# Kernel optimization log

Hardware: AMD Instinct MI355X
Metric: run time of the kernel (lower is better)

The kernel has to match this reference:

```python
import jax, jax.numpy as jnp
import numpy as np

D_MODEL = 1024
N_HEADS = 16
D_K = D_MODEL // N_HEADS
THETA = 10000.0
NEG_INF = -1e30


def _rope_tables(token_positions, d_k, theta=THETA):
    # freqs[t, i] = t / theta**(2i/d_k), i in [0, d_k/2)
    exponent = jnp.arange(0, d_k, 2, dtype=jnp.float32)  # [d_k/2]
    inv_freq = 1.0 / theta ** (exponent / d_k)
    freqs = token_positions.astype(jnp.float32)[:, None] * inv_freq[None, :]  # [s, d_k/2]
    return jnp.cos(freqs), jnp.sin(freqs)


def _apply_rope(x, cos, sin):
    # x: [..., s, d_k]; interleaved pair rotation (pairs are (x[2i], x[2i+1]))
    x1 = x[..., 0::2]
    x2 = x[..., 1::2]
    r1 = x1 * cos - x2 * sin
    r2 = x1 * sin + x2 * cos
    return jnp.stack([r1, r2], axis=-1).reshape(x.shape)


def setup_inputs() -> dict:
    key = jax.random.key(0)
    ks = jax.random.split(key, 5)
    b, s = 2, 2048
    scale = np.sqrt(2.0 / (D_MODEL + D_MODEL))
    return {
        "x": jax.random.normal(ks[0], (b, s, D_MODEL), dtype=jnp.float32),
        "Wq": jax.random.normal(ks[1], (D_MODEL, D_MODEL), dtype=jnp.float32) * scale,
        "Wk": jax.random.normal(ks[2], (D_MODEL, D_MODEL), dtype=jnp.float32) * scale,
        "Wv": jax.random.normal(ks[3], (D_MODEL, D_MODEL), dtype=jnp.float32) * scale,
        "Wo": jax.random.normal(ks[4], (D_MODEL, D_MODEL), dtype=jnp.float32) * scale,
        "token_positions": jnp.arange(s, dtype=jnp.int64 if jax.config.jax_enable_x64 else jnp.int32),
    }


def reference(x, Wq, Wk, Wv, Wo, token_positions):
    b, s, _ = x.shape
    # QKV projections: weight stored [in, out]
    q = jnp.einsum('bsi,io->bso', x, Wq)
    k = jnp.einsum('bsi,io->bso', x, Wk)
    v = jnp.einsum('bsi,io->bso', x, Wv)
    # split heads: [b, h, s, d_k]
    q = q.reshape(b, s, N_HEADS, D_K).transpose(0, 2, 1, 3)
    k = k.reshape(b, s, N_HEADS, D_K).transpose(0, 2, 1, 3)
    v = v.reshape(b, s, N_HEADS, D_K).transpose(0, 2, 1, 3)
    # RoPE
    cos, sin = _rope_tables(token_positions, D_K)
    q = _apply_rope(q, cos, sin)
    k = _apply_rope(k, cos, sin)
    # causal attention with full materialized scores (faithful to source)
    scores = jnp.einsum('bhid,bhjd->bhij', q, k) / jnp.sqrt(jnp.float32(D_K))
    mask = jnp.tril(jnp.ones((s, s), dtype=bool))
    scores = jnp.where(mask, scores, NEG_INF)
    probs = jax.nn.softmax(scores, axis=-1)
    out = jnp.einsum('bhij,bhjd->bhid', probs, v)
    out = out.transpose(0, 2, 1, 3).reshape(b, s, D_MODEL)
    return jnp.einsum('bsi,io->bso', out, Wo)
```

## Files before the change

### kernel.cpp

```cpp
#include <hip/hip_runtime.h>
#include <cmath>

#define S_LEN 2048
#define DMODEL 1024
#define NHEADS 16
#define DK 64
#define BATCH 2
#define MTOT (BATCH * S_LEN)

using short8 = __attribute__((ext_vector_type(8))) short;
using floatx4 = __attribute__((ext_vector_type(4))) float;

__device__ __forceinline__ unsigned short f2b(float f) {
    union { float f; unsigned u; } v; v.f = f;
    unsigned r = v.u + 0x7fff + ((v.u >> 16) & 1);
    return (unsigned short)(r >> 16);
}

__device__ __forceinline__ void gload16(const void* g, void* l) {
    __builtin_amdgcn_global_load_lds(
        (const __attribute__((address_space(1))) unsigned int*)g,
        (__attribute__((address_space(3))) unsigned int*)l, 16, 0, 0);
}

__global__ void rope_tables_k(const int* __restrict__ tokpos,
                              float* __restrict__ ct, float* __restrict__ st) {
    int idx = blockIdx.x * blockDim.x + threadIdx.x;
    int si = idx >> 5;
    int ip = idx & 31;
    float pos = (float)tokpos[si];
    float inv_freq = powf(10000.0f, -(float)(2 * ip) / 64.0f);
    float ang = pos * inv_freq;
    ct[idx] = cosf(ang);
    st[idx] = sinf(ang);
}

__global__ __launch_bounds__(256) void cast_x_k(const float* __restrict__ x,
                                                unsigned short* __restrict__ xb) {
    int i = (blockIdx.x * 256 + threadIdx.x) * 8;
    float4 a = *(const float4*)(x + i);
    float4 b = *(const float4*)(x + i + 4);
    short8 o;
    o[0] = f2b(a.x); o[1] = f2b(a.y); o[2] = f2b(a.z); o[3] = f2b(a.w);
    o[4] = f2b(b.x); o[5] = f2b(b.y); o[6] = f2b(b.z); o[7] = f2b(b.w);
    *(short8*)(xb + i) = o;
}

__global__ __launch_bounds__(256) void trans_w_k(
    const float* W0, const float* W1, const float* W2, const float* W3,
    unsigned short* T0, unsigned short* T1, unsigned short* T2, unsigned short* T3) {
    __shared__ float t[64][65];
    int z = blockIdx.z;
    const float* W = z == 0 ? W0 : z == 1 ? W1 : z == 2 ? W2 : W3;
    unsigned short* T = z == 0 ? T0 : z == 1 ? T1 : z == 2 ? T2 : T3;
    const bool perm = (z < 2);
    int n0 = blockIdx.x * 64, k0 = blockIdx.y * 64;
    int rr = threadIdx.x >> 6, cc = threadIdx.x & 63;
#pragma unroll
    for (int r = 0; r < 16; r++) {
        int row = r * 4 + rr;
        t[row][cc] = W[(size_t)(k0 + row) * DMODEL + n0 + cc];
    }
    __syncthreads();
#pragma unroll
    for (int r = 0; r < 16; r++) {
        int row = r * 4 + rr;
        int drow = perm ? (((row & 1) ? 32 : 0) + (row >> 1)) : row;
        T[(size_t)(n0 + drow) * DMODEL + k0 + cc] = f2b(t[cc][row]);
    }
}

__global__ __launch_bounds__(256) void vtrans_k(const unsigned short* __restrict__ V,
                                                unsigned short* __restrict__ Vt) {
    __shared__ unsigned short t[64][72];
    const int tid = threadIdx.x;
    const int s0 = blockIdx.x * 64, d0 = blockIdx.y * 64;
    const int bb = s0 >> 11;
#pragma unroll
    for (int it = 0; it < 4; it++) {
        int e = (it * 256 + tid) * 4;
        int r = e >> 6, c = e & 63;
        *(ushort4*)&t[r][c] = *(const ushort4*)(V + (size_t)(s0 + r) * DMODEL + d0 + c);
    }
    __syncthreads();
#pragma unroll
    for (int it = 0; it < 4; it++) {
        int e = (it * 256 + tid) * 4;
        int r = e >> 6, c = e & 63;
        ushort4 v;
        v.x = t[c + 0][r]; v.y = t[c + 1][r];
        v.z = t[c + 2][r]; v.w = t[c + 3][r];
        *(ushort4*)(Vt + (size_t)(bb * 1024 + d0 + r) * S_LEN + (s0 & (S_LEN - 1)) + c) = v;
    }
}

__global__ __launch_bounds__(256) void mm_k(
    const unsigned short* __restrict__ A,
    const unsigned short* __restrict__ Bt0, const unsigned short* __restrict__ Bt1,
    const unsigned short* __restrict__ Bt2,
    void* C0, void* C1, void* C2,
    const float* __restrict__ ct, const float* __restrict__ st, int kind) {
    __shared__ __align__(16) unsigned short blob[8192];

    const int z = blockIdx.z;
    const unsigned short* Bt = z == 0 ? Bt0 : z == 1 ? Bt1 : Bt2;
    void* C = z == 0 ? C0 : z == 1 ? C1 : C2;
    const int mode = (kind == 1) ? 0 : (z == 2 ? 3 : 1);

    const int tid = threadIdx.x;
    const int w = tid >> 6, lane = tid & 63;
    const int l15 = lane & 15, quad = lane >> 4;
    const int wr = w >> 1, wc = w & 1;
    const int m0 = blockIdx.y * 128, n0 = blockIdx.x * 128;

    floatx4 acc[4][4];
#pragma unroll
    for (int i = 0; i < 4; i++)
#pragma unroll
        for (int j = 0; j < 4; j++) acc[i][j] = (floatx4){0.f, 0.f, 0.f, 0.f};

    for (int k0 = 0; k0 < DMODEL; k0 += 32) {
        if (k0) __syncthreads();
#pragma unroll
        for (int it = 0; it < 4; it++) {
            int g = it * 4 + w;
            const unsigned short* gp;
            if (g < 8)
                gp = A + (size_t)(m0 + g * 16 + l15) * DMODEL + k0 + (lane >> 4) * 8;
            else
                gp = Bt + (size_t)(n0 + (g - 8) * 16 + l15) * DMODEL + k0 + (lane >> 4) * 8;
            gload16(gp, (char*)blob + g * 1024);
        }
        __syncthreads();

        short8 af[4], bfr[4];
#pragma unroll
        for (int i = 0; i < 4; i++)
            af[i] = *(const short8*)((char*)blob + ((wr * 4 + i) * 64 + lane) * 16);
#pragma unroll
        for (int j = 0; j < 4; j++)
            bfr[j] = *(const short8*)((char*)blob + 8192 + ((wc * 4 + j) * 64 + lane) * 16);
#pragma unroll
        for (int i = 0; i < 4; i++)
#pragma unroll
            for (int j = 0; j < 4; j++)
                acc[i][j] = __builtin_amdgcn_mfma_f32_16x16x32_bf16(af[i], bfr[j], acc[i][j], 0, 0, 0);
    }

#pragma unroll
    for (int i = 0; i < 4; i++) {
        const int rowb = m0 + wr * 64 + i * 16 + quad * 4;
        if (mode == 0) {
            float* Cf = (float*)C;
#pragma unroll
            for (int j = 0; j < 4; j++) {
                int colb = n0 + wc * 64 + j * 16 + l15;
#pragma unroll
                for (int r = 0; r < 4; r++)
                    Cf[(size_t)(rowb + r) * DMODEL + colb] = acc[i][j][r];
            }
        } else if (mode == 1) {
            unsigned short* Cb = (unsigned short*)C;
#pragma unroll
            for (int jh = 0; jh < 2; jh++) {
                int ip = jh * 16 + l15;
                int cole = n0 + wc * 64 + jh * 16 + l15;
#pragma unroll
                for (int r = 0; r < 4; r++) {
                    int row = rowb + r;
                    int si = row & (S_LEN - 1);
                    float c = ct[si * 32 + ip];
                    float s = st[si * 32 + ip];
                    float e = acc[i][jh][r];
                    float od = acc[i][jh + 2][r];
                    Cb[(size_t)row * DMODEL + cole] = f2b(e * c - od * s);
                    Cb[(size_t)row * DMODEL + cole + 32] = f2b(e * s + od * c);
                }
            }
        } else {
            unsigned short* Cb = (unsigned short*)C;
#pragma unroll
            for (int j = 0; j < 4; j++) {
                int colb = n0 + wc * 64 + j * 16 + l15;
#pragma unroll
                for (int r = 0; r < 4; r++)
                    Cb[(size_t)(rowb + r) * DMODEL + colb] = f2b(acc[i][j][r]);
            }
        }
    }
}

__global__ __launch_bounds__(256) void attn_k(const unsigned short* __restrict__ Q,
                                              const unsigned short* __restrict__ K,
                                              const unsigned short* __restrict__ Vt,
                                              unsigned short* __restrict__ O) {
    __shared__ __align__(16) unsigned short Kblob[2][4096];
    __shared__ __align__(16) unsigned short Vblob[2][4096];
    __shared__ __align__(16) unsigned short Ps[4][16 * 72];

    const int tid = threadIdx.x;
    const int w = tid >> 6, lane = tid & 63;
    const int l15 = lane & 15, quad = lane >> 4;
    const int idx = blockIdx.x;
    const int qt = 31 - (idx >> 5);
    const int bh = idx & 31;
    const int bb = bh >> 4, h = bh & 15;
    const int qbase = qt * 64 + w * 16;
    const int qrow = qbase + l15;

    const size_t qoff = (size_t)(bb * S_LEN + qbase + l15) * DMODEL + h * DK;
    short8 aq0 = *(const short8*)(Q + qoff + quad * 8);
    short8 aq1 = *(const short8*)(Q + qoff + 32 + quad * 8);

    floatx4 o[4];
#pragma unroll
    for (int f = 0; f < 4; f++) o[f] = (floatx4){0.f, 0.f, 0.f, 0.f};
    float mv = -1e30f, lv = 0.f;

    const unsigned short* Kb = K + (size_t)(bb * S_LEN) * DMODEL + h * DK;
    const unsigned short* Vb = Vt + (size_t)(bb * 1024 + h * DK) * S_LEN;
    unsigned short* ps = &Ps[w][0];

    auto stage = [&](int b, int kb) {
#pragma unroll
        for (int it = 0; it < 4; it++) {
            int g = it * 4 + w;
            if (g < 8) {
                const unsigned short* gp =
                    Kb + (size_t)(kb + (g >> 1) * 16 + l15) * DMODEL + (g & 1) * 32 + quad * 8;
                gload16(gp, (char*)&Kblob[b][0] + g * 1024);
            } else {
                int gv = g - 8;
                const unsigned short* gp =
                    Vb + (size_t)((gv >> 1) * 16 + l15) * S_LEN + kb + (gv & 1) * 32 + quad * 8;
                gload16(gp, (char*)&Vblob[b][0] + gv * 1024);
            }
        }
    };

    const int nkt = qt + 1;
    stage(0, 0);
    for (int kt = 0; kt < nkt; kt++) {
        const int b = kt & 1;
        const int kb = kt * 64;
        __syncthreads();
        if (kt + 1 < nkt) stage(b ^ 1, (kt + 1) * 64);

        const unsigned short* kbb = &Kblob[b][0];
        floatx4 c[4];
#pragma unroll
        for (int g = 0; g < 4; g++) {
            short8 kf0 = *(const short8*)(kbb + (g * 2 + 0) * 512 + lane * 8);
            short8 kf1 = *(const short8*)(kbb + (g * 2 + 1) * 512 + lane * 8);
            floatx4 t = {0.f, 0.f, 0.f, 0.f};
            t = __builtin_amdgcn_mfma_f32_16x16x32_bf16(kf0, aq0, t, 0, 0, 0);
            c[g] = __builtin_amdgcn_mfma_f32_16x16x32_bf16(kf1, aq1, t, 0, 0, 0);
        }

        float sv[16];
#pragma unroll
        for (int g = 0; g < 4; g++)
#pragma unroll
            for (int r = 0; r < 4; r++) {
                int key = kb + g * 16 + quad * 4 + r;
                sv[g * 4 + r] = (key <= qrow) ? c[g][r] * 0.125f : -1e30f;
            }
        float mx = sv[0];
#pragma unroll
        for (int i = 1; i < 16; i++) mx = fmaxf(mx, sv[i]);
        mx = fmaxf(mx, __shfl_xor(mx, 16));
        mx = fmaxf(mx, __shfl_xor(mx, 32));
        float mnew = fmaxf(mv, mx);
        float alpha = __expf(mv - mnew);
        mv = mnew;
        float p[16], psum = 0.f;
#pragma unroll
        for (int i = 0; i < 16; i++) {
            p[i] = __expf(sv[i] - mnew);
            psum += p[i];
        }
        lv = lv * alpha + psum;

#pragma unroll
        for (int g = 0; g < 4; g++) {
            ushort4 pk;
            pk.x = f2b(p[g * 4 + 0]); pk.y = f2b(p[g * 4 + 1]);
            pk.z = f2b(p[g * 4 + 2]); pk.w = f2b(p[g * 4 + 3]);
            *(ushort4*)(ps + l15 * 72 + g * 16 + quad * 4) = pk;
        }
#pragma unroll
        for (int f = 0; f < 4; f++) {
            o[f][0] *= alpha; o[f][1] *= alpha;
            o[f][2] *= alpha; o[f][3] *= alpha;
        }
        short8 pf0 = *(const short8*)(ps + l15 * 72 + quad * 8);
        short8 pf1 = *(const short8*)(ps + l15 * 72 + 32 + quad * 8);
        const unsigned short* vbb = &Vblob[b][0];
#pragma unroll
        for (int f = 0; f < 4; f++) {
            short8 vf0 = *(const short8*)(vbb + (f * 2 + 0) * 512 + lane * 8);
            short8 vf1 = *(const short8*)(vbb + (f * 2 + 1) * 512 + lane * 8);
            o[f] = __builtin_amdgcn_mfma_f32_16x16x32_bf16(vf0, pf0, o[f], 0, 0, 0);
            o[f] = __builtin_amdgcn_mfma_f32_16x16x32_bf16(vf1, pf1, o[f], 0, 0, 0);
        }
    }

    lv += __shfl_xor(lv, 16);
    lv += __shfl_xor(lv, 32);
    float inv = 1.0f / lv;
    __syncthreads();
#pragma unroll
    for (int f = 0; f < 4; f++) {
        ushort4 pk;
        pk.x = f2b(o[f][0] * inv);
        pk.y = f2b(o[f][1] * inv);
        pk.z = f2b(o[f][2] * inv);
        pk.w = f2b(o[f][3] * inv);
        *(ushort4*)(ps + l15 * 72 + f * 16 + quad * 4) = pk;
    }
    short8 r0 = *(const short8*)(ps + l15 * 72 + quad * 8);
    short8 r1 = *(const short8*)(ps + l15 * 72 + 32 + quad * 8);
    size_t obase = (size_t)(bb * S_LEN + qbase + l15) * DMODEL + h * DK;
    *(short8*)(O + obase + quad * 8) = r0;
    *(short8*)(O + obase + 32 + quad * 8) = r1;
}

extern "C" void kernel_launch(void* const* d_in, const int* in_sizes, int n_in,
                              void* d_out, int out_size, void* d_ws,
                              size_t ws_size, hipStream_t stream) {
    const float* x = (const float*)d_in[0];
    const float* Wq = (const float*)d_in[1];
    const float* Wk = (const float*)d_in[2];
    const float* Wv = (const float*)d_in[3];
    const float* Wo = (const float*)d_in[4];
    const int* tokpos = (const int*)d_in[5];
    float* out = (float*)d_out;

    const size_t MD = (size_t)MTOT * DMODEL;
    const size_t WD = (size_t)DMODEL * DMODEL;
    unsigned short* xb = (unsigned short*)d_ws;
    unsigned short* Wqt = xb + MD;
    unsigned short* Wkt = Wqt + WD;
    unsigned short* Wvt = Wkt + WD;
    unsigned short* Wot = Wvt + WD;
    unsigned short* Q = Wot + WD;
    unsigned short* K = Q + MD;
    unsigned short* V = K + MD;
    unsigned short* Vt = V + MD;
    float* ct = (float*)(Vt + MD);
    float* st = ct + S_LEN * 32;
    unsigned short* O = V;

    rope_tables_k<<<dim3((S_LEN * 32) / 256), dim3(256), 0, stream>>>(tokpos, ct, st);
    cast_x_k<<<dim3(MD / 2048), dim3(256), 0, stream>>>(x, xb);
    trans_w_k<<<dim3(16, 16, 4), dim3(256), 0, stream>>>(Wq, Wk, Wv, Wo, Wqt, Wkt, Wvt, Wot);

    mm_k<<<dim3(8, 32, 3), dim3(256), 0, stream>>>(xb, Wqt, Wkt, Wvt,
                                                   (void*)Q, (void*)K, (void*)V, ct, st, 0);
    vtrans_k<<<dim3(64, 16), dim3(256), 0, stream>>>(V, Vt);
    attn_k<<<dim3(1024), dim3(256), 0, stream>>>(Q, K, Vt, O);
    mm_k<<<dim3(8, 32, 1), dim3(256), 0, stream>>>(O, Wot, Wot, Wot,
                                                   (void*)out, (void*)out, (void*)out, ct, st, 1);
}
```

Baseline: 224.0 us.

## Merge prep kernels, deepen GEMM K-step, and widen attention blocks to 128 queries

Three preprocessing kernels (rope tables, x cast, weight transpose) are folded into one launch that branches on block index, removing launch overhead. The GEMM stages a 64-wide K slice per iteration instead of 32, halving barriers and doubling LDS per block. Attention blocks grow to 512 threads covering 128 query rows, so each staged K/V tile is shared by eight waves instead of four. The cost is lower occupancy from the larger LDS and blocks, coarser causal load balance across 512 blocks, and the hidden attention loop body must handle diagonal masking for the 128-row tile correctly.

```diff
diff --git a/kernel.cpp b/kernel.cpp
--- a/kernel.cpp
+++ b/kernel.cpp
@@ -23,50 +23,51 @@
         (__attribute__((address_space(3))) unsigned int*)l, 16, 0, 0);
 }
 
-__global__ void rope_tables_k(const int* __restrict__ tokpos,
-                              float* __restrict__ ct, float* __restrict__ st) {
-    int idx = blockIdx.x * blockDim.x + threadIdx.x;
-    int si = idx >> 5;
-    int ip = idx & 31;
-    float pos = (float)tokpos[si];
-    float inv_freq = powf(10000.0f, -(float)(2 * ip) / 64.0f);
-    float ang = pos * inv_freq;
-    ct[idx] = cosf(ang);
-    st[idx] = sinf(ang);
-}
-
-__global__ __launch_bounds__(256) void cast_x_k(const float* __restrict__ x,
-                                                unsigned short* __restrict__ xb) {
-    int i = (blockIdx.x * 256 + threadIdx.x) * 8;
-    float4 a = *(const float4*)(x + i);
-    float4 b = *(const float4*)(x + i + 4);
-    short8 o;
-    o[0] = f2b(a.x); o[1] = f2b(a.y); o[2] = f2b(a.z); o[3] = f2b(a.w);
-    o[4] = f2b(b.x); o[5] = f2b(b.y); o[6] = f2b(b.z); o[7] = f2b(b.w);
-    *(short8*)(xb + i) = o;
-}
-
-__global__ __launch_bounds__(256) void trans_w_k(
+__global__ __launch_bounds__(256) void prep_k(
+    const float* __restrict__ x, unsigned short* __restrict__ xb,
+    const int* __restrict__ tokpos, float* __restrict__ ct, float* __restrict__ st,
     const float* W0, const float* W1, const float* W2, const float* W3,
     unsigned short* T0, unsigned short* T1, unsigned short* T2, unsigned short* T3) {
     __shared__ float t[64][65];
-    int z = blockIdx.z;
-    const float* W = z == 0 ? W0 : z == 1 ? W1 : z == 2 ? W2 : W3;
-    unsigned short* T = z == 0 ? T0 : z == 1 ? T1 : z == 2 ? T2 : T3;
-    const bool perm = (z < 2);
-    int n0 = blockIdx.x * 64, k0 = blockIdx.y * 64;
-    int rr = threadIdx.x >> 6, cc = threadIdx.x & 63;
-#pragma unroll
-    for (int r = 0; r < 16; r++) {
-        int row = r * 4 + rr;
-        t[row][cc] = W[(size_t)(k0 + row) * DMODEL + n0 + cc];
-    }
-    __syncthreads();
-#pragma unroll
-    for (int r = 0; r < 16; r++) {
-        int row = r * 4 + rr;
-        int drow = perm ? (((row & 1) ? 32 : 0) + (row >> 1)) : row;
-        T[(size_t)(n0 + drow) * DMODEL + k0 + cc] = f2b(t[cc][row]);
+    const int b = blockIdx.x;
+    if (b < 2048) {
+        int i = (b * 256 + threadIdx.x) * 8;
+        float4 a = *(const float4*)(x + i);
+        float4 bb = *(const float4*)(x + i + 4);
+        short8 o;
+        o[0] = f2b(a.x); o[1] = f2b(a.y); o[2] = f2b(a.z); o[3] = f2b(a.w);
+        o[4] = f2b(bb.x); o[5] = f2b(bb.y); o[6] = f2b(bb.z); o[7] = f2b(bb.w);
+        *(short8*)(xb + i) = o;
+    } else if (b < 2304) {
+        int idx = (b - 2048) * 256 + threadIdx.x;
+        int si = idx >> 5;
+        int ip = idx & 31;
+        float pos = (float)tokpos[si];
+        float inv_freq = powf(10000.0f, -(float)(2 * ip) / 64.0f);
+        float ang = pos * inv_freq;
+        ct[idx] = cosf(ang);
+        st[idx] = sinf(ang);
+    } else {
+        int id = b - 2304;
+        int z = id >> 8;
+        int bx = id & 15, by = (id >> 4) & 15;
+        const float* W = z == 0 ? W0 : z == 1 ? W1 : z == 2 ? W2 : W3;
+        unsigned short* T = z == 0 ? T0 : z == 1 ? T1 : z == 2 ? T2 : T3;
+        const bool perm = (z < 2);
+        int n0 = bx * 64, k0 = by * 64;
+        int rr = threadIdx.x >> 6, cc = threadIdx.x & 63;
+#pragma unroll
+        for (int r = 0; r < 16; r++) {
+            int row = r * 4 + rr;
+            t[row][cc] = W[(size_t)(k0 + row) * DMODEL + n0 + cc];
+        }
+        __syncthreads();
+#pragma unroll
+        for (int r = 0; r < 16; r++) {
+            int row = r * 4 + rr;
+            int drow = perm ? (((row & 1) ? 32 : 0) + (row >> 1)) : row;
+            T[(size_t)(n0 + drow) * DMODEL + k0 + cc] = f2b(t[cc][row]);
+        }
     }
 }
 
@@ -100,7 +101,7 @@
     const unsigned short* __restrict__ Bt2,
     void* C0, void* C1, void* C2,
     const float* __restrict__ ct, const float* __restrict__ st, int kind) {
-    __shared__ __align__(16) unsigned short blob[8192];
+    __shared__ __align__(16) unsigned short blob[16384];
 
     const int z = blockIdx.z;
     const unsigned short* Bt = z == 0 ? Bt0 : z == 1 ? Bt1 : Bt2;
@@ -119,32 +120,37 @@
 #pragma unroll
         for (int j = 0; j < 4; j++) acc[i][j] = (floatx4){0.f, 0.f, 0.f, 0.f};
 
-    for (int k0 = 0; k0 < DMODEL; k0 += 32) {
+    for (int k0 = 0; k0 < DMODEL; k0 += 64) {
         if (k0) __syncthreads();
 #pragma unroll
-        for (int it = 0; it < 4; it++) {
+        for (int it = 0; it < 8; it++) {
             int g = it * 4 + w;
             const unsigned short* gp;
-            if (g < 8)
-                gp = A + (size_t)(m0 + g * 16 + l15) * DMODEL + k0 + (lane >> 4) * 8;
-            else
-                gp = Bt + (size_t)(n0 + (g - 8) * 16 + l15) * DMODEL + k0 + (lane >> 4) * 8;
+            if (g < 16)
+                gp = A + (size_t)(m0 + (g & 7) * 16 + l15) * DMODEL + k0 + (g >> 3) * 32 + quad * 8;
+            else {
+                int gb = g - 16;
+                gp = Bt + (size_t)(n0 + (gb & 7) * 16 + l15) * DMODEL + k0 + (gb >> 3) * 32 + quad * 8;
+            }
             gload16(gp, (char*)blob + g * 1024);
         }
         __syncthreads();
 
-        short8 af[4], bfr[4];
-#pragma unroll
-        for (int i = 0; i < 4; i++)
-            af[i] = *(const short8*)((char*)blob + ((wr * 4 + i) * 64 + lane) * 16);
-#pragma unroll
-        for (int j = 0; j < 4; j++)
-            bfr[j] = *(const short8*)((char*)blob + 8192 + ((wc * 4 + j) * 64 + lane) * 16);
-#pragma unroll
-        for (int i = 0; i < 4; i++)
+#pragma unroll
+        for (int h = 0; h < 2; h++) {
+            short8 af[4], bfr[4];
+#pragma unroll
+            for (int i = 0; i < 4; i++)
+                af[i] = *(const short8*)((char*)blob + ((h * 8 + wr * 4 + i) * 64 + lane) * 16);
 #pragma unroll
             for (int j = 0; j < 4; j++)
-                acc[i][j] = __builtin_amdgcn_mfma_f32_16x16x32_bf16(af[i], bfr[j], acc[i][j], 0, 0, 0);
+                bfr[j] = *(const short8*)((char*)blob + 16384 + ((h * 8 + wc * 4 + j) * 64 + lane) * 16);
+#pragma unroll
+            for (int i = 0; i < 4; i++)
+#pragma unroll
+                for (int j = 0; j < 4; j++)
+                    acc[i][j] = __builtin_amdgcn_mfma_f32_16x16x32_bf16(af[i], bfr[j], acc[i][j], 0, 0, 0);
+        }
     }
 
 #pragma unroll
@@ -190,22 +196,22 @@
     }
 }
 
-__global__ __launch_bounds__(256) void attn_k(const unsigned short* __restrict__ Q,
+__global__ __launch_bounds__(512) void attn_k(const unsigned short* __restrict__ Q,
                                               const unsigned short* __restrict__ K,
                                               const unsigned short* __restrict__ Vt,
                                               unsigned short* __restrict__ O) {
     __shared__ __align__(16) unsigned short Kblob[2][4096];
     __shared__ __align__(16) unsigned short Vblob[2][4096];
-    __shared__ __align__(16) unsigned short Ps[4][16 * 72];
+    __shared__ __align__(16) unsigned short Ps[8][16 * 72];
 
     const int tid = threadIdx.x;
     const int w = tid >> 6, lane = tid & 63;
     const int l15 = lane & 15, quad = lane >> 4;
     const int idx = blockIdx.x;
-    const int qt = 31 - (idx >> 5);
+    const int qt = 15 - (idx >> 5);
     const int bh = idx & 31;
     const int bb = bh >> 4, h = bh & 15;
-    const int qbase = qt * 64 + w * 16;
+    const int qbase = qt * 128 + w * 16;
     const int qrow = qbase + l15;
 
     const size_t qoff = (size_t)(bb * S_LEN + qbase + l15) * DMODEL + h * DK;
@@ -223,8 +229,8 @@
 
     auto stage = [&](int b, int kb) {
 #pragma unroll
-        for (int it = 0; it < 4; it++) {
-            int g = it * 4 + w;
+        for (int it = 0; it < 2; it++) {
+            int g = it * 8 + w;
             if (g < 8) {
                 const unsigned short* gp =
                     Kb + (size_t)(kb + (g >> 1) * 16 + l15) * DMODEL + (g & 1) * 32 + quad * 8;
@@ -238,7 +244,7 @@
         }
     };
 
-    const int nkt = qt + 1;
+    const int nkt = 2 * qt + 2;
     stage(0, 0);
     for (int kt = 0; kt < nkt; kt++) {
         const int b = kt & 1;
@@ -351,14 +357,13 @@
     float* st = ct + S_LEN * 32;
     unsigned short* O = V;
 
-    rope_tables_k<<<dim3((S_LEN * 32) / 256), dim3(256), 0, stream>>>(tokpos, ct, st);
-    cast_x_k<<<dim3(MD / 2048), dim3(256), 0, stream>>>(x, xb);
-    trans_w_k<<<dim3(16, 16, 4), dim3(256), 0, stream>>>(Wq, Wk, Wv, Wo, Wqt, Wkt, Wvt, Wot);
+    prep_k<<<dim3(3328), dim3(256), 0, stream>>>(x, xb, tokpos, ct, st,
+                                                 Wq, Wk, Wv, Wo, Wqt, Wkt, Wvt, Wot);
 
     mm_k<<<dim3(8, 32, 3), dim3(256), 0, stream>>>(xb, Wqt, Wkt, Wvt,
                                                    (void*)Q, (void*)K, (void*)V, ct, st, 0);
     vtrans_k<<<dim3(64, 16), dim3(256), 0, stream>>>(V, Vt);
-    attn_k<<<dim3(1024), dim3(256), 0, stream>>>(Q, K, Vt, O);
+    attn_k<<<dim3(512), dim3(512), 0, stream>>>(Q, K, Vt, O);
     mm_k<<<dim3(8, 32, 1), dim3(256), 0, stream>>>(O, Wot, Wot, Wot,
                                                    (void*)out, (void*)out, (void*)out, ct, st, 1);
 }
```

New measurement: 222.3 us. About the same (-0.7%).
